# Kernel tuning notes

Hardware: AMD Instinct MI355X
Metric: run time of the kernel (lower is better)

The kernel has to match this reference:

```python
import jax, jax.numpy as jnp
import numpy as np

NEG = jnp.float32(-1e30)


def setup_inputs() -> dict:
    key = jax.random.key(0)
    k1, k2, k3, k4 = jax.random.split(key, 4)
    B, T, K, Dmax = 16, 2048, 256, 64
    # per-timestep emission log-likelihoods (would come from self.pdf.log_prob(X))
    log_B = jax.random.normal(k1, (B, T, K), dtype=jnp.float32)
    # normalized log-prob buffers, matching _init_buffers (Dirichlet-ish -> log_softmax)
    pi_logits = jax.nn.log_softmax(jax.random.normal(k2, (K,), dtype=jnp.float32))
    # SEMI transition constraint: no self transitions (diagonal = -inf), rows normalized
    A_raw = jax.random.normal(k3, (K, K), dtype=jnp.float32)
    A_raw = jnp.where(jnp.eye(K, dtype=bool), NEG, A_raw)
    A_logits = jax.nn.log_softmax(A_raw, axis=1)
    D_logits = jax.nn.log_softmax(jax.random.normal(k4, (K, Dmax), dtype=jnp.float32), axis=1)
    return {"log_B": log_B, "pi_logits": pi_logits, "A_logits": A_logits, "D_logits": D_logits}


def _hsmm_forward(logb, cumb, pi_logits, A_logits, D_logits):
    """Explicit-duration HSMM forward pass (log-space) for one sequence.

    alpha_t(j) = logsumexp_{d=1..Dmax} [ a_{t-d}(j) + D_j(d) + sum_{s=t-d+1..t} b_j(o_s) ]
    a_tau(j)   = logsumexp_i alpha_tau(i) + A_{ij},  a_0 = pi.
    Segment emission sums via cumsum: cumb[t] - cumb[t-d].
    Carry a rolling buffer buf[d-1, j] = a_{t-d}(j) - cumb[t-d](j).
    """
    K = pi_logits.shape[0]
    Dmax = D_logits.shape[1]
    Dt = D_logits.T  # [Dmax, K]
    # t=1: only d=1 valid, buf[0] = a_0 - cumb[0] = pi - 0
    buf0 = jnp.full((Dmax, K), NEG, dtype=logb.dtype).at[0].set(pi_logits)

    def step(buf, cumb_t):
        # alpha_t(j): logsumexp over durations d
        alpha = jax.nn.logsumexp(buf + Dt, axis=0) + cumb_t          # [K]
        # incoming mass for a segment starting at t+1
        a_in = jax.nn.logsumexp(alpha[:, None] + A_logits, axis=0)   # [K]
        buf = jnp.roll(buf, 1, axis=0).at[0].set(a_in - cumb_t)
        return buf, alpha

    _, alphas = jax.lax.scan(step, buf0, cumb)  # alphas: [T, K]
    loglik = jax.nn.logsumexp(alphas[-1])
    return loglik, alphas


def reference(log_B, pi_logits, A_logits, D_logits):
    cumB = jnp.cumsum(log_B, axis=1)  # [B, T, K]
    loglik, alphas = jax.vmap(_hsmm_forward, in_axes=(0, 0, None, None, None))(
        log_B, cumB, pi_logits, A_logits, D_logits)
    return loglik, alphas
```

## Files before the change

kernel.cpp:

```cpp
#include <hip/hip_runtime.h>
#include <cstddef>

#define LOG2E 1.4426950408889634f
#define LN2   0.6931471805599453f

typedef float    f32x2 __attribute__((ext_vector_type(2)));
typedef float    f32x4 __attribute__((ext_vector_type(4)));
typedef _Float16 half8 __attribute__((ext_vector_type(8)));

constexpr int K_    = 256;
constexpr int T_    = 2048;
constexpr int DMAX_ = 64;
constexpr int B_    = 16;

__device__ __forceinline__ float fexp2(float x) { return __builtin_amdgcn_exp2f(x); }
__device__ __forceinline__ float flog2(float x) { return __builtin_amdgcn_logf(x); }
__device__ __forceinline__ float frcp (float x) { return __builtin_amdgcn_rcpf(x); }

__device__ __forceinline__ f32x2 xchg32(float x) {
    float a, b;
    asm("v_mov_b32 %0, %2\n\t"
        "v_mov_b32 %1, %2\n\t"
        "s_nop 1\n\t"
        "v_permlane32_swap_b32 %0, %1"
        : "=&v"(a), "=&v"(b)
        : "v"(x));
    return (f32x2){a, b};
}

template<int CTRL>
__device__ __forceinline__ float dpp_maxf(float x) {
    int m = __builtin_amdgcn_update_dpp(0, __builtin_bit_cast(int, x), CTRL, 0xF, 0xF, true);
    return fmaxf(x, __builtin_bit_cast(float, m));
}

__global__ __launch_bounds__(512)
__attribute__((amdgpu_waves_per_eu(2, 2)))
void hsmm_fwd_kernel(const float* __restrict__ logB,
                     const float* __restrict__ pi,
                     const float* __restrict__ A,
                     const float* __restrict__ D,
                     float* __restrict__ out)
{
    const int b    = blockIdx.x;
    const int tid  = threadIdx.x;
    const int w    = tid >> 6;
    const int lane = tid & 63;
    const int j    = (w << 5) | (lane & 31);
    const int q    = lane >> 5;

    alignas(16) __shared__ _Float16 lds_ph[2][K_];
    alignas(16) __shared__ float    lds_red[2][8];

    half8 Bf0[8], Bf1[8];
    {
        const int krow = (lane >> 4) * 8;
        const int n0   = (w << 5) + (lane & 15);
        #pragma unroll
        for (int kc = 0; kc < 8; ++kc) {
            #pragma unroll
            for (int jj = 0; jj < 8; ++jj) {
                const int k = kc * 32 + krow + jj;
                Bf0[kc][jj] = (_Float16)fexp2(A[(size_t)k * K_ + n0     ] * LOG2E);
                Bf1[kc][jj] = (_Float16)fexp2(A[(size_t)k * K_ + n0 + 16] * LOG2E);
            }
        }
    }
    f32x2 pDf[16];
    {
        const float* Dj = D + (size_t)j * DMAX_ + 32 * q;
        #pragma unroll
        for (int k = 0; k < 16; ++k)
            pDf[k] = (f32x2){ fexp2(Dj[2 * k] * LOG2E), fexp2(Dj[2 * k + 1] * LOG2E) };
    }

    f32x2 v[16];
    #pragma unroll
    for (int k = 0; k < 16; ++k) v[k] = (f32x2){0.0f, 0.0f};
    if (q == 0) v[0].x = 1.0f;
    float mcol     = pi[j] * LOG2E;
    float cumb     = 0.0f;
    float m_anchor = 0.0f;

    if (tid < 8) { lds_red[0][tid] = 0.0f; lds_red[1][tid] = 0.0f; }
    __syncthreads();

    const float* lb = logB + (size_t)b * T_ * K_ + j;
    float*       ao = out + 16 + (size_t)b * T_ * K_ + j;

    float bld0 = lb[0];
    float bld1 = lb[K_];
    float bld2 = lb[2 * K_];
    int   ldoff = 3 * K_;
    int   aoff  = 0;

    #pragma unroll 2
    for (int t = 0; t < T_; ++t) {
        const int s = t & 1;
        cumb = fmaf(bld0, LOG2E, cumb);

        const float argh = 0.5f * (cumb + mcol - m_anchor);
        const float ea   = fminf(fexp2(argh),  1.8e19f);
        const float ga   = fminf(fexp2(-argh), 1.8e19f);
        const float mac  = m_anchor - cumb;

        f32x2 s0 = {0.f,0.f}, s1 = {0.f,0.f}, s2 = {0.f,0.f}, s3 = {0.f,0.f};
        #pragma unroll
        for (int k = 0; k < 16; k += 4) {
            s0 = __builtin_elementwise_fma(v[k + 0], pDf[k + 0], s0);
            s1 = __builtin_elementwise_fma(v[k + 1], pDf[k + 1], s1);
            s2 = __builtin_elementwise_fma(v[k + 2], pDf[k + 2], s2);
            s3 = __builtin_elementwise_fma(v[k + 3], pDf[k + 3], s3);
        }
        f32x2 sp = (s0 + s1) + (s2 + s3);
        float Sl = sp.x + sp.y;
        f32x2 pr = xchg32(Sl);
        float S  = pr.x + pr.y;

        float p = fminf(S * ea * ea, 60000.0f);
        if (q == 0) lds_ph[s][j] = (_Float16)p;
        float alpha_l2 = cumb + mcol + flog2(S);

        asm volatile("s_waitcnt lgkmcnt(0)" ::: "memory");
        __builtin_amdgcn_sched_barrier(0);
        __builtin_amdgcn_s_barrier();
        __builtin_amdgcn_sched_barrier(0);

        bld0 = bld1; bld1 = bld2;
        bld2 = lb[ldoff];
        ldoff += (ldoff < (T_ - 1) * K_) ? K_ : 0;
        if (q == 0) ao[aoff] = alpha_l2 * LN2;
        aoff += K_;

        f32x4 r0 = ((const f32x4*)lds_red[s ^ 1])[0];
        f32x4 r1 = ((const f32x4*)lds_red[s ^ 1])[1];

        const _Float16* pb = lds_ph[s];
        const int fo = (lane >> 4) * 8;
        const f32x4 z = {0.f,0.f,0.f,0.f};
        f32x4 d0a = z, d0b = z, d1a = z, d1b = z;
        #pragma unroll
        for (int kc = 0; kc < 4; ++kc) {
            half8 af = *(const half8*)(pb + kc * 32 + fo);
            d0a = __builtin_amdgcn_mfma_f32_16x16x32_f16(af, Bf0[kc], d0a, 0, 0, 0);
            d1a = __builtin_amdgcn_mfma_f32_16x16x32_f16(af, Bf1[kc], d1a, 0, 0, 0);
        }
        #pragma unroll
        for (int kc = 4; kc < 8; ++kc) {
            half8 af = *(const half8*)(pb + kc * 32 + fo);
            d0b = __builtin_amdgcn_mfma_f32_16x16x32_f16(af, Bf0[kc], d0b, 0, 0, 0);
            d1b = __builtin_amdgcn_mfma_f32_16x16x32_f16(af, Bf1[kc], d1b, 0, 0, 0);
        }
        float sva = d0a.x + d0b.x;
        float svb = d1a.x + d1b.x;
        float mySmv = (lane & 16) ? svb : sva;

        float m_next = fmaxf(fmaxf(fmaxf(r0.x, r0.y), fmaxf(r0.z, r0.w)),
                             fmaxf(fmaxf(r1.x, r1.y), fmaxf(r1.z, r1.w)));

        float mx = fmaxf(sva, svb);
        mx = dpp_maxf<0x121>(mx);
        mx = dpp_maxf<0x122>(mx);
        mx = dpp_maxf<0x124>(mx);
        mx = dpp_maxf<0x128>(mx);
        if (lane == 0) lds_red[s][w] = m_anchor + flog2(fmaxf(mx, 1e-30f));

        float nv0 = mySmv * ga * ga;
        float rsc = frcp(fmaxf(nv0, 1.0f));
        float nv  = fminf(nv0, 1.0f);
        mcol = fmaxf(mcol, mac + flog2(mySmv));
        f32x2 hp  = xchg32(v[15].y);
        float oth = (hp.x == v[15].y) ? hp.y : hp.x;
        float hand = oth * rsc;
        #pragma unroll
        for (int k = 15; k >= 1; --k) {
            v[k].y = v[k].x * rsc;
            v[k].x = v[k - 1].y * rsc;
        }
        v[0].y = v[0].x * rsc;
        v[0].x = (q == 0) ? nv : hand;
        if (t + 1 < T_) m_anchor = m_next;
    }

    if (tid < 64) {
        const _Float16* lp = lds_ph[(T_ - 1) & 1];
        float sf = (float)lp[tid] + (float)lp[tid + 64]
                 + (float)lp[tid + 128] + (float)lp[tid + 192];
        #pragma unroll
        for (int off = 1; off < 64; off <<= 1)
            sf += __shfl_xor(sf, off, 64);
        if (tid == 0) out[b] = (m_anchor + flog2(sf)) * LN2;
    }
}

extern "C" void kernel_launch(void* const* d_in, const int* in_sizes, int n_in,
                              void* d_out, int out_size, void* d_ws, size_t ws_size,
                              hipStream_t stream) {
    const float* logB = (const float*)d_in[0];
    const float* pi   = (const float*)d_in[1];
    const float* A    = (const float*)d_in[2];
    const float* D    = (const float*)d_in[3];
    float* out = (float*)d_out;
    (void)in_sizes; (void)n_in; (void)d_ws; (void)ws_size; (void)out_size;

    hipLaunchKernelGGL(hsmm_fwd_kernel, dim3(B_), dim3(512), 0, stream,
                       logB, pi, A, D, out);
}
```

Measured before the change: 1.691 ms.

## Precompute duration dot product off critical path using shifted duration weights

The per-step duration reduction S no longer waits on the head value produced after the MFMA/rescale chain. The kernel now applies the buffer shift with the previous step's rescale factor and computes the 31-term dot product with pre-shifted duration weights. This work happens after the barrier, in parallel with the MFMA stage. At the next step S is formed as rsc*ds + hv*pD1, a single FMA, which shortens the serial dependency chain before the LDS write and barrier. The cost is an extra 32-register weight array and a reordering of the shift relative to the rescale.

```diff
diff --git a/kernel.cpp b/kernel.cpp
--- a/kernel.cpp
+++ b/kernel.cpp
@@ -67,20 +67,33 @@
         }
     }
     f32x2 pDf[16];
+    f32x2 pDf_s[16];
     {
         const float* Dj = D + (size_t)j * DMAX_ + 32 * q;
         #pragma unroll
         for (int k = 0; k < 16; ++k)
             pDf[k] = (f32x2){ fexp2(Dj[2 * k] * LOG2E), fexp2(Dj[2 * k + 1] * LOG2E) };
-    }
+        #pragma unroll
+        for (int k = 0; k < 16; ++k) {
+            float sx = fexp2(Dj[2 * k + 1] * LOG2E);
+            float sy = (k == 15) ? ((q == 0) ? fexp2(Dj[32] * LOG2E) : 0.0f)
+                                 : fexp2(Dj[2 * k + 2] * LOG2E);
+            pDf_s[k] = (f32x2){ sx, sy };
+        }
+    }
+    const float pD1 = fexp2(D[(size_t)j * DMAX_] * LOG2E);
 
     f32x2 v[16];
     #pragma unroll
     for (int k = 0; k < 16; ++k) v[k] = (f32x2){0.0f, 0.0f};
-    if (q == 0) v[0].x = 1.0f;
     float mcol     = pi[j] * LOG2E;
     float cumb     = 0.0f;
     float m_anchor = 0.0f;
+
+    float rsc_p   = 1.0f;
+    float hv      = 1.0f;
+    float hvpd    = pD1;
+    float ds_full = 0.0f;
 
     if (tid < 8) { lds_red[0][tid] = 0.0f; lds_red[1][tid] = 0.0f; }
     __syncthreads();
@@ -102,24 +115,13 @@
         const float argh = 0.5f * (cumb + mcol - m_anchor);
         const float ea   = fminf(fexp2(argh),  1.8e19f);
         const float ga   = fminf(fexp2(-argh), 1.8e19f);
+        const float ea2  = ea * ea;
+        const float ga2  = ga * ga;
         const float mac  = m_anchor - cumb;
 
-        f32x2 s0 = {0.f,0.f}, s1 = {0.f,0.f}, s2 = {0.f,0.f}, s3 = {0.f,0.f};
-        #pragma unroll
-        for (int k = 0; k < 16; k += 4) {
-            s0 = __builtin_elementwise_fma(v[k + 0], pDf[k + 0], s0);
-            s1 = __builtin_elementwise_fma(v[k + 1], pDf[k + 1], s1);
-            s2 = __builtin_elementwise_fma(v[k + 2], pDf[k + 2], s2);
-            s3 = __builtin_elementwise_fma(v[k + 3], pDf[k + 3], s3);
-        }
-        f32x2 sp = (s0 + s1) + (s2 + s3);
-        float Sl = sp.x + sp.y;
-        f32x2 pr = xchg32(Sl);
-        float S  = pr.x + pr.y;
-
-        float p = fminf(S * ea * ea, 60000.0f);
+        const float S = fmaf(rsc_p, ds_full, hvpd);
+        float p = fminf(S * ea2, 60000.0f);
         if (q == 0) lds_ph[s][j] = (_Float16)p;
-        float alpha_l2 = cumb + mcol + flog2(S);
 
         asm volatile("s_waitcnt lgkmcnt(0)" ::: "memory");
         __builtin_amdgcn_sched_barrier(0);
@@ -129,11 +131,35 @@
         bld0 = bld1; bld1 = bld2;
         bld2 = lb[ldoff];
         ldoff += (ldoff < (T_ - 1) * K_) ? K_ : 0;
-        if (q == 0) ao[aoff] = alpha_l2 * LN2;
+        if (q == 0) ao[aoff] = (cumb + mcol + flog2(S)) * LN2;
         aoff += K_;
 
         f32x4 r0 = ((const f32x4*)lds_red[s ^ 1])[0];
         f32x4 r1 = ((const f32x4*)lds_red[s ^ 1])[1];
+
+        f32x2 hp  = xchg32(v[15].y);
+        float oth = (hp.x == v[15].y) ? hp.y : hp.x;
+        float hand = oth * rsc_p;
+        #pragma unroll
+        for (int k = 15; k >= 1; --k) {
+            v[k].y = v[k].x * rsc_p;
+            v[k].x = v[k - 1].y * rsc_p;
+        }
+        v[0].y = v[0].x * rsc_p;
+        v[0].x = (q == 0) ? hv : hand;
+
+        f32x2 s0 = {0.f,0.f}, s1 = {0.f,0.f}, s2 = {0.f,0.f}, s3 = {0.f,0.f};
+        #pragma unroll
+        for (int k = 0; k < 16; k += 4) {
+            s0 = __builtin_elementwise_fma(v[k + 0], pDf_s[k + 0], s0);
+            s1 = __builtin_elementwise_fma(v[k + 1], pDf_s[k + 1], s1);
+            s2 = __builtin_elementwise_fma(v[k + 2], pDf_s[k + 2], s2);
+            s3 = __builtin_elementwise_fma(v[k + 3], pDf_s[k + 3], s3);
+        }
+        f32x2 sp = (s0 + s1) + (s2 + s3);
+        float Sl = sp.x + sp.y;
+        f32x2 pr = xchg32(Sl);
+        float dsn = pr.x + pr.y;
 
         const _Float16* pb = lds_ph[s];
         const int fo = (lane >> 4) * 8;
@@ -165,20 +191,12 @@
         mx = dpp_maxf<0x128>(mx);
         if (lane == 0) lds_red[s][w] = m_anchor + flog2(fmaxf(mx, 1e-30f));
 
-        float nv0 = mySmv * ga * ga;
-        float rsc = frcp(fmaxf(nv0, 1.0f));
-        float nv  = fminf(nv0, 1.0f);
-        mcol = fmaxf(mcol, mac + flog2(mySmv));
-        f32x2 hp  = xchg32(v[15].y);
-        float oth = (hp.x == v[15].y) ? hp.y : hp.x;
-        float hand = oth * rsc;
-        #pragma unroll
-        for (int k = 15; k >= 1; --k) {
-            v[k].y = v[k].x * rsc;
-            v[k].x = v[k - 1].y * rsc;
-        }
-        v[0].y = v[0].x * rsc;
-        v[0].x = (q == 0) ? nv : hand;
+        float nv0 = mySmv * ga2;
+        rsc_p = frcp(fmaxf(nv0, 1.0f));
+        hv    = fminf(nv0, 1.0f);
+        hvpd  = hv * pD1;
+        mcol  = fmaxf(mcol, mac + flog2(mySmv));
+        ds_full = dsn;
         if (t + 1 < T_) m_anchor = m_next;
     }
 
```

Measured after the change: 1.968 ms. 1.16x slower.

## Reorder duration layout for packed shifts and update max anchor every two steps

Applied to the files above, without the earlier changes.

The per-lane duration layout is reindexed so each f32x2 holds durations i and 16+i. The rolling-buffer shift then becomes one packed multiply per register pair instead of scalar cross-element moves. The loop is manually unrolled into even and odd halves: the wave-level max reduction and LDS write happen only on even steps, and the anchor update happens only on odd steps, using a single LDS buffer. This trims work on the serial per-timestep critical path. The risk is larger dynamic range between anchor updates, which the existing clamps must absorb. An extra register move in the lane-swap helper is also removed.

```diff
diff --git a/kernel.cpp b/kernel.cpp
--- a/kernel.cpp
+++ b/kernel.cpp
@@ -18,12 +18,11 @@
 __device__ __forceinline__ float frcp (float x) { return __builtin_amdgcn_rcpf(x); }
 
 __device__ __forceinline__ f32x2 xchg32(float x) {
-    float a, b;
-    asm("v_mov_b32 %0, %2\n\t"
-        "v_mov_b32 %1, %2\n\t"
+    float a = x, b;
+    asm("v_mov_b32 %1, %2\n\t"
         "s_nop 1\n\t"
         "v_permlane32_swap_b32 %0, %1"
-        : "=&v"(a), "=&v"(b)
+        : "+v"(a), "=&v"(b)
         : "v"(x));
     return (f32x2){a, b};
 }
@@ -50,7 +49,7 @@
     const int q    = lane >> 5;
 
     alignas(16) __shared__ _Float16 lds_ph[2][K_];
-    alignas(16) __shared__ float    lds_red[2][8];
+    alignas(16) __shared__ float    lds_red[8];
 
     half8 Bf0[8], Bf1[8];
     {
@@ -70,19 +69,19 @@
     {
         const float* Dj = D + (size_t)j * DMAX_ + 32 * q;
         #pragma unroll
-        for (int k = 0; k < 16; ++k)
-            pDf[k] = (f32x2){ fexp2(Dj[2 * k] * LOG2E), fexp2(Dj[2 * k + 1] * LOG2E) };
+        for (int i = 0; i < 16; ++i)
+            pDf[i] = (f32x2){ fexp2(Dj[i] * LOG2E), fexp2(Dj[16 + i] * LOG2E) };
     }
 
     f32x2 v[16];
     #pragma unroll
-    for (int k = 0; k < 16; ++k) v[k] = (f32x2){0.0f, 0.0f};
+    for (int i = 0; i < 16; ++i) v[i] = (f32x2){0.0f, 0.0f};
     if (q == 0) v[0].x = 1.0f;
     float mcol     = pi[j] * LOG2E;
     float cumb     = 0.0f;
     float m_anchor = 0.0f;
 
-    if (tid < 8) { lds_red[0][tid] = 0.0f; lds_red[1][tid] = 0.0f; }
+    if (tid < 8) lds_red[tid] = 0.0f;
     __syncthreads();
 
     const float* lb = logB + (size_t)b * T_ * K_ + j;
@@ -94,9 +93,7 @@
     int   ldoff = 3 * K_;
     int   aoff  = 0;
 
-    #pragma unroll 2
-    for (int t = 0; t < T_; ++t) {
-        const int s = t & 1;
+    auto body = [&](int t, int s, bool even) __attribute__((always_inline)) {
         cumb = fmaf(bld0, LOG2E, cumb);
 
         const float argh = 0.5f * (cumb + mcol - m_anchor);
@@ -119,7 +116,6 @@
 
         float p = fminf(S * ea * ea, 60000.0f);
         if (q == 0) lds_ph[s][j] = (_Float16)p;
-        float alpha_l2 = cumb + mcol + flog2(S);
 
         asm volatile("s_waitcnt lgkmcnt(0)" ::: "memory");
         __builtin_amdgcn_sched_barrier(0);
@@ -129,11 +125,14 @@
         bld0 = bld1; bld1 = bld2;
         bld2 = lb[ldoff];
         ldoff += (ldoff < (T_ - 1) * K_) ? K_ : 0;
-        if (q == 0) ao[aoff] = alpha_l2 * LN2;
+        if (q == 0) ao[aoff] = (cumb + mcol + flog2(S)) * LN2;
         aoff += K_;
 
-        f32x4 r0 = ((const f32x4*)lds_red[s ^ 1])[0];
-        f32x4 r1 = ((const f32x4*)lds_red[s ^ 1])[1];
+        f32x4 r0, r1;
+        if (!even) {
+            r0 = ((const f32x4*)lds_red)[0];
+            r1 = ((const f32x4*)lds_red)[1];
+        }
 
         const _Float16* pb = lds_ph[s];
         const int fo = (lane >> 4) * 8;
@@ -155,31 +154,41 @@
         float svb = d1a.x + d1b.x;
         float mySmv = (lane & 16) ? svb : sva;
 
-        float m_next = fmaxf(fmaxf(fmaxf(r0.x, r0.y), fmaxf(r0.z, r0.w)),
-                             fmaxf(fmaxf(r1.x, r1.y), fmaxf(r1.z, r1.w)));
-
-        float mx = fmaxf(sva, svb);
-        mx = dpp_maxf<0x121>(mx);
-        mx = dpp_maxf<0x122>(mx);
-        mx = dpp_maxf<0x124>(mx);
-        mx = dpp_maxf<0x128>(mx);
-        if (lane == 0) lds_red[s][w] = m_anchor + flog2(fmaxf(mx, 1e-30f));
+        float m_next = 0.0f;
+        if (even) {
+            float mx = fmaxf(sva, svb);
+            mx = dpp_maxf<0x121>(mx);
+            mx = dpp_maxf<0x122>(mx);
+            mx = dpp_maxf<0x124>(mx);
+            mx = dpp_maxf<0x128>(mx);
+            if (lane == 0) lds_red[w] = m_anchor + flog2(fmaxf(mx, 1e-30f));
+        } else {
+            float m1 = fmaxf(fmaxf(r0.x, r0.y), fmaxf(r0.z, r0.w));
+            float m2 = fmaxf(fmaxf(r1.x, r1.y), fmaxf(r1.z, r1.w));
+            m_next = fmaxf(m1, m2);
+        }
 
         float nv0 = mySmv * ga * ga;
         float rsc = frcp(fmaxf(nv0, 1.0f));
         float nv  = fminf(nv0, 1.0f);
         mcol = fmaxf(mcol, mac + flog2(mySmv));
+
         f32x2 hp  = xchg32(v[15].y);
         float oth = (hp.x == v[15].y) ? hp.y : hp.x;
-        float hand = oth * rsc;
-        #pragma unroll
-        for (int k = 15; k >= 1; --k) {
-            v[k].y = v[k].x * rsc;
-            v[k].x = v[k - 1].y * rsc;
-        }
-        v[0].y = v[0].x * rsc;
-        v[0].x = (q == 0) ? nv : hand;
-        if (t + 1 < T_) m_anchor = m_next;
+        float p15lo = v[15].x;
+        f32x2 rp = { rsc, rsc };
+        #pragma unroll
+        for (int k = 15; k >= 1; --k)
+            v[k] = v[k - 1] * rp;
+        v[0].y = p15lo * rsc;
+        v[0].x = (q == 0) ? nv : oth * rsc;
+
+        if (!even && t + 1 < T_) m_anchor = m_next;
+    };
+
+    for (int t = 0; t < T_; t += 2) {
+        body(t,     0, true );
+        body(t + 1, 1, false);
     }
 
     if (tid < 64) {
```

New measurement: 1.440 ms (median of 3 runs). -14.8%, faster.
